# Optimization experiments

Hardware: AMD Instinct MI355X
Metric: run time of the kernel (lower is better)

The kernel has to match this reference:

```python
import jax, jax.numpy as jnp
import numpy as np

N_CONCEPTS = 32
KMEANS_ITERS = 10   # fixed Lloyd iterations (stand-in for fit-to-convergence)
CC_ITERS = 20       # label-propagation + pointer-jumping iterations (>= ~2*log2(N))


def setup_inputs() -> dict:
    key = jax.random.key(0)
    k1, k2, k3, k4 = jax.random.split(key, 4)
    B, N, F = 16, 512, 256
    x = jax.random.normal(k1, (B, N, F), dtype=jnp.float32)
    # sparse symmetric 0/1 adjacency, no self loops, avg degree ~20
    u = jax.random.uniform(k2, (B, N, N))
    a = (u < 0.02).astype(jnp.float32)
    adj = jnp.clip(a + jnp.swapaxes(a, 1, 2), 0.0, 1.0)
    adj = adj * (1.0 - jnp.eye(N, dtype=jnp.float32))
    mask = jnp.ones((B, N), dtype=bool)
    s = 1.0 / np.sqrt(F)
    W1 = jax.random.normal(k3, (F, F), jnp.float32) * s
    b1 = jnp.zeros((F,), jnp.float32)
    W2 = jax.random.normal(k4, (F, F), jnp.float32) * s
    b2 = jnp.zeros((F,), jnp.float32)
    return {"x": x, "adj": adj, "mask": mask, "W1": W1, "b1": b1, "W2": W2, "b2": b2}


def _gcn(x, adj, mask, W, b):
    # DenseGCNConv: D^-1/2 (A+I) D^-1/2 (X W) + b, masked
    N = x.shape[1]
    h = x @ W
    a = adj + jnp.eye(N, dtype=adj.dtype)
    d = jnp.clip(a.sum(-1), 1.0, None) ** -0.5
    a = d[:, :, None] * a * d[:, None, :]
    out = jnp.einsum('bij,bjf->bif', a, h) + b
    return jnp.where(mask[:, :, None], out, 0.0)


def _kmeans_fit_predict(pts, k):
    # Lloyd iterations, euclidean; deterministic init = first k points
    cent = pts[:k]
    p2 = (pts * pts).sum(-1)
    for _ in range(KMEANS_ITERS):
        d2 = p2[:, None] - 2.0 * pts @ cent.T + (cent * cent).sum(-1)[None]
        assign = jnp.argmin(d2, -1)
        sums = jax.ops.segment_sum(pts, assign, num_segments=k)
        cnt = jax.ops.segment_sum(jnp.ones_like(p2), assign, num_segments=k)
        cent = jnp.where(cnt[:, None] > 0, sums / jnp.maximum(cnt, 1.0)[:, None], cent)
    d2 = p2[:, None] - 2.0 * pts @ cent.T + (cent * cent).sum(-1)[None]
    return jnp.argmin(d2, -1)


def _components(adj_same, mask):
    # connected components of same-concept subgraph; returns 1-based cluster ids (0 = masked)
    B, N, _ = adj_same.shape
    idx = jnp.arange(N)
    labels = jnp.broadcast_to(idx[None, :], (B, N))
    A = adj_same > 0

    def step(lab, _):
        nb = jnp.where(A, lab[:, None, :], N)        # [B,N,N] neighbor labels
        lab = jnp.minimum(lab, nb.min(-1))           # hook to min neighbor
        lab = jnp.take_along_axis(lab, lab, axis=1)  # pointer jump
        lab = jnp.take_along_axis(lab, lab, axis=1)
        return lab, None

    labels, _ = jax.lax.scan(step, labels, None, length=CC_ITERS)
    is_root = mask & (labels == idx[None, :])
    ids = jnp.cumsum(is_root.astype(jnp.int32), axis=1)   # consecutive ids, 1-based at roots
    assign = jnp.take_along_axis(ids, labels, axis=1)
    return jnp.where(mask, assign, 0)


def _forward(x, adj, mask, W1, b1, W2, b2):
    B, N, F = x.shape
    h = jax.nn.relu(_gcn(x, adj, mask, W1, b1))
    h = jax.nn.relu(_gcn(h, adj, mask, W2, b2))
    # mask is all-true -> x[mask] is a flat reshape
    pts = jax.lax.stop_gradient(h.reshape(B * N, F))
    concepts = _kmeans_fit_predict(pts, N_CONCEPTS).reshape(B, N)
    adj_same = jnp.where(concepts[:, :, None] == concepts[:, None, :], adj, 0.0)
    assignments = _components(adj_same, mask)           # [B,N] in {0..N}
    seg_sum = jax.vmap(lambda v, s: jax.ops.segment_sum(v, s, num_segments=N + 1))
    x_new = seg_sum(h, assignments)[:, 1:, :]           # drop reserved cluster 0
    seg_max = jax.vmap(lambda v, s: jax.ops.segment_max(v, s, num_segments=N + 1))
    adj_r = jnp.maximum(seg_max(adj, assignments), 0.0)[:, 1:, :]                      # pool rows
    adj_new = jnp.maximum(seg_max(jnp.swapaxes(adj_r, 1, 2), assignments), 0.0)[:, 1:, :]
    adj_new = jnp.swapaxes(adj_new, 1, 2)                                              # pool cols
    num_clusters = assignments.max(-1)
    mask_new = jnp.arange(N)[None, :] < num_clusters[:, None]
    return x_new, adj_new, concepts, h, mask_new


def reference(x, adj, mask, W1, b1, W2, b2):
    return _forward(x, adj, mask, W1, b1, W2, b2)
```

## Files before the change

### kernel.cpp

```cpp
#include <hip/hip_runtime.h>
#include <cstdint>
#include <cstddef>

#define BB 16
#define NN 512
#define FF 256
#define NC 32
#define KITERS 10
#define CCITERS 20
#define MAXD 96
#define FMAXD 64

typedef __attribute__((ext_vector_type(4))) double double4_t;

__global__ __launch_bounds__(64) void build_adjbits(const float* __restrict__ adj,
                                                    unsigned long long* __restrict__ adjbits,
                                                    double* __restrict__ dinv,
                                                    unsigned short* __restrict__ nbr,
                                                    int* __restrict__ degv) {
  int i = blockIdx.x, b = blockIdx.y, lane = threadIdx.x;
  const float* row = adj + ((size_t)(b * NN + i)) * NN;
  unsigned long long lmask = (1ULL << lane) - 1ULL;
  int base = 0;
#pragma unroll
  for (int q = 0; q < 8; ++q) {
    bool pred = (row[q * 64 + lane] != 0.0f);
    unsigned long long m = __ballot(pred ? 1 : 0);
    if (lane == 0) adjbits[((size_t)(b * NN + i)) * 8 + q] = m;
    if (pred) {
      int pos = base + __popcll(m & lmask);
      if (pos < MAXD) nbr[((size_t)(b * NN + i)) * MAXD + pos] = (unsigned short)(q * 64 + lane);
    }
    base += __popcll(m);
  }
  if (lane == 0) {
    degv[b * NN + i] = base;
    double tot = (double)base + 1.0;
    dinv[b * NN + i] = 1.0 / sqrt(tot);
  }
}

__global__ __launch_bounds__(256) void gemm_scale(const float* __restrict__ X,
                                                  const float* __restrict__ W,
                                                  const double* __restrict__ dinv,
                                                  float* __restrict__ Y) {
  __shared__ float As[16][68];
  __shared__ float Bs[16][64];
  int bm = blockIdx.x, bn = blockIdx.y, b = blockIdx.z;
  int tid = threadIdx.x;
  int tx = tid & 15, ty = tid >> 4;
  const float* Xb = X + (size_t)b * NN * FF;
  float* Yb = Y + (size_t)b * NN * FF;
  double acc[4][4] = {};
  for (int kt = 0; kt < FF; kt += 16) {
    {
      int m = tid >> 2, kq = (tid & 3) * 4;
      const float4 v = *(const float4*)&Xb[(size_t)(bm * 64 + m) * FF + kt + kq];
      As[kq + 0][m] = v.x; As[kq + 1][m] = v.y; As[kq + 2][m] = v.z; As[kq + 3][m] = v.w;
    }
    {
      int k = tid >> 4, n4 = (tid & 15) * 4;
      *(float4*)&Bs[k][n4] = *(const float4*)&W[(size_t)(kt + k) * FF + bn * 64 + n4];
    }
    __syncthreads();
#pragma unroll
    for (int k = 0; k < 16; ++k) {
      float4 a = *(const float4*)&As[k][ty * 4];
      float4 bv = *(const float4*)&Bs[k][tx * 4];
      double ax = a.x, ay = a.y, az = a.z, aw = a.w;
      double bx = bv.x, by = bv.y, bz = bv.z, bw = bv.w;
      acc[0][0] += ax * bx; acc[0][1] += ax * by; acc[0][2] += ax * bz; acc[0][3] += ax * bw;
      acc[1][0] += ay * bx; acc[1][1] += ay * by; acc[1][2] += ay * bz; acc[1][3] += ay * bw;
      acc[2][0] += az * bx; acc[2][1] += az * by; acc[2][2] += az * bz; acc[2][3] += az * bw;
      acc[3][0] += aw * bx; acc[3][1] += aw * by; acc[3][2] += aw * bz; acc[3][3] += aw * bw;
    }
    __syncthreads();
  }
#pragma unroll
  for (int i = 0; i < 4; ++i) {
    int row = bm * 64 + ty * 4 + i;
    double di = dinv[b * NN + row];
    float4 v;
    v.x = (float)(di * acc[i][0]); v.y = (float)(di * acc[i][1]);
    v.z = (float)(di * acc[i][2]); v.w = (float)(di * acc[i][3]);
    *(float4*)&Yb[(size_t)row * FF + bn * 64 + tx * 4] = v;
  }
}

__global__ __launch_bounds__(256) void spmv_relu(const float* __restrict__ Y,
                                                 const unsigned short* __restrict__ nbr,
                                                 const int* __restrict__ degv,
                                                 const unsigned long long* __restrict__ adjbits,
                                                 const double* __restrict__ dinv,
                                                 const float* __restrict__ bias,
                                                 float* __restrict__ H) {
  int i = blockIdx.x, b = blockIdx.y, f = threadIdx.x;
  int row = b * NN + i;
  const float* Yb = Y + (size_t)b * NN * FF;
  double z = (double)Yb[(size_t)i * FF + f];
  int deg = degv[row];
  if (deg <= MAXD) {
    const unsigned short* lst = nbr + (size_t)row * MAXD;
    int n = 0;
    for (; n + 4 <= deg; n += 4) {
      int j0 = lst[n], j1 = lst[n + 1], j2 = lst[n + 2], j3 = lst[n + 3];
      float v0 = Yb[(size_t)j0 * FF + f];
      float v1 = Yb[(size_t)j1 * FF + f];
      float v2 = Yb[(size_t)j2 * FF + f];
      float v3 = Yb[(size_t)j3 * FF + f];
      z += (double)v0; z += (double)v1; z += (double)v2; z += (double)v3;
    }
    for (; n < deg; ++n) z += (double)Yb[(size_t)lst[n] * FF + f];
  } else {
    const unsigned long long* brow = adjbits + (size_t)row * 8;
    for (int q = 0; q < 8; ++q) {
      unsigned long long bits = brow[q];
      while (bits) {
        int j = (q << 6) + __builtin_ctzll(bits);
        bits &= bits - 1;
        z += (double)Yb[(size_t)j * FF + f];
      }
    }
  }
  double h = dinv[row] * z + (double)bias[f];
  H[((size_t)row) * FF + f] = (h > 0.0) ? (float)h : 0.0f;
}

__global__ __launch_bounds__(256) void p2cent_kernel(const float* __restrict__ pts,
                                                     double* __restrict__ p2,
                                                     double* __restrict__ cent) {
  __shared__ double red[256];
  int p = blockIdx.x, t = threadIdx.x;
  double v = (double)pts[(size_t)p * FF + t];
  if (p < NC) cent[p * FF + t] = v;
  red[t] = v * v;
  __syncthreads();
  for (int s = 128; s; s >>= 1) { if (t < s) red[t] += red[t + s]; __syncthreads(); }
  if (t == 0) p2[p] = red[0];
}

__global__ __launch_bounds__(256) void kmeans_assign(const float* __restrict__ pts,
                                                     const double* __restrict__ cent,
                                                     const double* __restrict__ p2,
                                                     int* __restrict__ assignI,
                                                     double* __restrict__ part,
                                                     int* __restrict__ cntp,
                                                     float* __restrict__ conceptsF) {
  __shared__ float ps[32][260];
  __shared__ double csT[256][35];
  __shared__ double d2s[32][33];
  __shared__ double c2s[32];
  __shared__ double want[3];
  __shared__ double probe_raw[2][2];
  __shared__ int as[32];
  __shared__ int hyp;
  int g = blockIdx.x, tid = threadIdx.x;

  for (int r = 0; r < 32; ++r) ps[r][tid] = pts[(size_t)(g * 32 + r) * FF + tid];
  for (int rep = 0; rep < 32; ++rep) csT[tid][rep] = cent[rep * FF + tid];
  __syncthreads();

  if (tid < 32) {
    double s = 0.;
    for (int k = 0; k < FF; ++k) { double cv = csT[k][tid]; s += cv * cv; }
    c2s[tid] = s;
  }

  int lane = tid & 63, w = tid >> 6;
  int prow = (w >> 1) * 16, ccol = (w & 1) * 16;
  int r16 = lane & 15, kg = lane >> 4;
  double4_t acc = {0.0, 0.0, 0.0, 0.0};
  for (int kt = 0; kt < FF; kt += 4) {
    double a = (double)ps[prow + r16][kt + kg];
    double bv = csT[kt + kg][ccol + r16];
    acc = __builtin_amdgcn_mfma_f64_16x16x4f64(a, bv, acc, 0, 0, 0);
  }
  if (tid < 2) { probe_raw[tid][0] = acc[0]; probe_raw[tid][1] = acc[1]; }
  __syncthreads();

  if (tid < 192) {
    int pw = tid >> 6;
    int pr = (pw == 2) ? 1 : 0;
    int pc = (pw == 1) ? 1 : 0;
    double partial = 0.0;
#pragma unroll
    for (int kk = 0; kk < 4; ++kk)
      partial += (double)ps[pr][lane * 4 + kk] * csT[lane * 4 + kk][pc];
    for (int off = 32; off; off >>= 1) partial += __shfl_xor(partial, off, 64);
    if (lane == 0) want[pw] = partial;
  }
  __syncthreads();
  if (tid == 0) {
    double w00 = want[0], w01 = want[1], w10 = want[2];
    double m00 = probe_raw[0][0], mA = probe_raw[1][0], mB = probe_raw[0][1];
    auto near = [](double a, double b) { return fabs(a - b) <= 1e-9 * (1.0 + fabs(b)); };
    bool ok00 = near(m00, w00);
    bool h1 = ok00 && near(mA, w01) && near(mB, w10);
    bool h2 = ok00 && near(mB, w01) && near(mA, w10);
    hyp = h1 ? 0 : (h2 ? 1 : 2);
  }
  __syncthreads();
  int hh = hyp;
  if (hh == 0) {
#pragma unroll
    for (int ii = 0; ii < 4; ++ii) {
      int row = prow + kg * 4 + ii, col = ccol + r16;
      d2s[row][col] = (p2[g * 32 + row] - 2.0 * acc[ii]) + c2s[col];
    }
  } else if (hh == 1) {
#pragma unroll
    for (int ii = 0; ii < 4; ++ii) {
      int row = prow + r16, col = ccol + kg * 4 + ii;
      d2s[row][col] = (p2[g * 32 + row] - 2.0 * acc[ii]) + c2s[col];
    }
  }
  __syncthreads();
  if (hh == 2) {
    int p0 = tid >> 4, c0 = tid & 15;
    double a00 = 0., a01 = 0., a10 = 0., a11 = 0.;
    for (int k = 0; k < FF; ++k) {
      double pa = (double)ps[p0][k], pb = (double)ps[p0 + 16][k];
      double ca = csT[k][c0], cb = csT[k][c0 + 16];
      a00 += pa * ca; a01 += pa * cb; a10 += pb * ca; a11 += pb * cb;
    }
    double pp0 = p2[g * 32 + p0], pp1 = p2[g * 32 + p0 + 16];
    double cc0 = c2s[c0], cc1 = c2s[c0 + 16];
    d2s[p0][c0]           = (pp0 - 2.0 * a00) + cc0;
    d2s[p0][c0 + 16]      = (pp0 - 2.0 * a01) + cc1;
    d2s[p0 + 16][c0]      = (pp1 - 2.0 * a10) + cc0;
    d2s[p0 + 16][c0 + 16] = (pp1 - 2.0 * a11) + cc1;
  }
  __syncthreads();

  if (tid < 32) {
    double m = d2s[tid][0];
    int idx = 0;
    for (int c = 1; c < 32; ++c) {
      double v = d2s[tid][c];
      if (v < m) { m = v; idx = c; }
    }
    as[tid] = idx;
    assignI[g * 32 + tid] = idx;
    if (conceptsF) conceptsF[g * 32 + tid] = (float)idx;
  }
  double* accm = &csT[0][0];
  for (int r = 0; r < 32; ++r) accm[r * 258 + tid] = 0.0;
  __syncthreads();
  for (int r = 0; r < 32; ++r) { int s = as[r]; accm[s * 258 + tid] += (double)ps[r][tid]; }
  for (int r = 0; r < 32; ++r) part[((size_t)r * 256 + g) * FF + tid] = accm[r * 258 + tid];
  if (tid < 32) {
    int c = 0;
    for (int r = 0; r < 32; ++r) c += (as[r] == tid) ? 1 : 0;
    cntp[tid * 256 + g] = c;
  }
}

__global__ __launch_bounds__(256) void kmeans_update(const double* __restrict__ part,
                                                     const int* __restrict__ cntp,
                                                     double* __restrict__ cent) {
  __shared__ double red[8][33];
  __shared__ int cred[256];
  int k = blockIdx.x, fc = blockIdx.y;
  int tid = threadIdx.x;
  int fl = tid & 31, gl = tid >> 5;
  int f = fc * 32 + fl;
  double s = 0.;
  for (int gg = 0; gg < 32; ++gg) {
    int g = gl + gg * 8;
    s += part[((size_t)k * 256 + g) * FF + f];
  }
  red[gl][fl] = s;
  cred[tid] = cntp[k * 256 + tid];
  __syncthreads();
  for (int q = 128; q; q >>= 1) { if (tid < q) cred[tid] += cred[tid + q]; __syncthreads(); }
  if (gl == 0) {
    double acc = 0.;
    for (int q = 0; q < 8; ++q) acc += red[q][fl];
    int cnt = cred[0];
    double v = (cnt > 0) ? (acc / (double)cnt) : cent[k * FF + f];
    cent[k * FF + f] = v;
  }
}

__global__ __launch_bounds__(64) void build_bits(const unsigned long long* __restrict__ adjbits,
                                                 const int* __restrict__ concepts,
                                                 unsigned short* __restrict__ flistT,
                                                 int* __restrict__ fdegv) {
  int i = blockIdx.x, b = blockIdx.y, lane = threadIdx.x;
  int ci = concepts[b * NN + i];
  unsigned long long lmask = (1ULL << lane) - 1ULL;
  int base = 0;
#pragma unroll
  for (int q = 0; q < 8; ++q) {
    unsigned long long wbits = adjbits[((size_t)(b * NN + i)) * 8 + q];
    bool pred = ((wbits >> lane) & 1ULL) && (concepts[b * NN + q * 64 + lane] == ci);
    unsigned long long m = __ballot(pred ? 1 : 0);
    if (pred) {
      int pos = base + __popcll(m & lmask);
      if (pos < FMAXD) flistT[((size_t)b * FMAXD + pos) * NN + i] = (unsigned short)(q * 64 + lane);
    }
    base += __popcll(m);
  }
  if (lane == 0) fdegv[b * NN + i] = base;
}

__global__ __launch_bounds__(512) void components_kernel(const unsigned short* __restrict__ flistT,
                                                         const int* __restrict__ fdegv,
                                                         int* __restrict__ comp,
                                                         float* __restrict__ maskF) {
  __shared__ unsigned short LT[FMAXD][512];
  __shared__ int lab[512];
  __shared__ int ids[512];
  int b = blockIdx.x, t = threadIdx.x;
  for (int n = 0; n < FMAXD; ++n) LT[n][t] = flistT[((size_t)b * FMAXD + n) * NN + t];
  int fd = fdegv[b * NN + t];
  if (fd > FMAXD) fd = FMAXD;
  lab[t] = t;
  __syncthreads();
  for (int it = 0; it < CCITERS; ++it) {
    int old = lab[t];
    int m = old;
    for (int n = 0; n < fd; ++n) m = min(m, lab[LT[n][t]]);
    __syncthreads();
    lab[t] = m;
    __syncthreads();
    int a = lab[m];
    __syncthreads();
    lab[t] = a;
    __syncthreads();
    int a2 = lab[a];
    __syncthreads();
    lab[t] = a2;
    int changed = (a2 != old) ? 1 : 0;
    if (__syncthreads_or(changed) == 0) break;
  }
  if (t == 0) {
    int run = 0;
    for (int i = 0; i < 512; ++i) { run += (lab[i] == i) ? 1 : 0; ids[i] = run; }
  }
  __syncthreads();
  comp[b * NN + t] = ids[lab[t]];
  maskF[b * NN + t] = (t < ids[511]) ? 1.0f : 0.0f;
}

__global__ __launch_bounds__(256) void xnew_kernel(const float* __restrict__ H,
                                                   const int* __restrict__ comp,
                                                   float* __restrict__ xnew) {
  int i = blockIdx.x, b = blockIdx.y, f = threadIdx.x;
  int s = comp[b * NN + i] - 1;
  atomicAdd(&xnew[((size_t)(b * NN + s)) * FF + f], H[((size_t)(b * NN + i)) * FF + f]);
}

__global__ __launch_bounds__(64) void adjnew_kernel(const unsigned long long* __restrict__ adjbits,
                                                    const int* __restrict__ comp,
                                                    float* __restrict__ out) {
  int b = blockIdx.y, lane = threadIdx.x;
  int i = blockIdx.x * 8 + (lane >> 3);
  int q = lane & 7;
  unsigned long long bits = adjbits[((size_t)(b * NN + i)) * 8 + q];
  if (!bits) return;
  int si = comp[b * NN + i] - 1;
  float* ob = out + (size_t)b * NN * NN;
  while (bits) {
    int j = (q << 6) + __builtin_ctzll(bits);
    bits &= bits - 1;
    int sj = comp[b * NN + j] - 1;
    ob[(size_t)si * NN + sj] = 1.0f;
  }
}

extern "C" void kernel_launch(void* const* d_in, const int* in_sizes, int n_in,
                              void* d_out, int out_size, void* d_ws, size_t ws_size,
                              hipStream_t stream) {
  (void)in_sizes; (void)n_in; (void)out_size; (void)ws_size;
  const float* x   = (const float*)d_in[0];
  const float* adj = (const float*)d_in[1];
  const float* W1 = (const float*)d_in[3];
  const float* b1 = (const float*)d_in[4];
  const float* W2 = (const float*)d_in[5];
  const float* b2 = (const float*)d_in[6];

  float* out = (float*)d_out;
  float* xnew      = out;
  float* adjnew    = out + 2097152;
  float* conceptsF = out + 6291456;
  float* hout      = out + 6299648;
  float* maskF     = out + 8396800;

  char* ws = (char*)d_ws;
  double* dinv = (double*)(ws + 0);
  float*  y    = (float*)(ws + 65536);
  float*  h1   = (float*)(ws + 8454144);
  double* cent = (double*)(ws + 16842752);
  double* p2   = (double*)(ws + 16908544);
  unsigned long long* adjbits = (unsigned long long*)(ws + 16974080);
  int* assignI = (int*)(ws + 17498368);
  int* cntp    = (int*)(ws + 17531136);
  int* comp    = (int*)(ws + 17563904);
  int* degv    = assignI;
  double* part = (double*)adjnew;
  unsigned short* nbr = (unsigned short*)xnew;
  unsigned short* flistT = (unsigned short*)h1;
  int* fdegv = (int*)(ws + 8454144 + 2097152);

  build_adjbits<<<dim3(NN, BB), 64, 0, stream>>>(adj, adjbits, dinv, nbr, degv);

  gemm_scale<<<dim3(8, 4, BB), 256, 0, stream>>>(x, W1, dinv, y);
  spmv_relu<<<dim3(NN, BB), 256, 0, stream>>>(y, nbr, degv, adjbits, dinv, b1, h1);
  gemm_scale<<<dim3(8, 4, BB), 256, 0, stream>>>(h1, W2, dinv, y);
  spmv_relu<<<dim3(NN, BB), 256, 0, stream>>>(y, nbr, degv, adjbits, dinv, b2, hout);

  hipMemsetAsync(xnew, 0, (size_t)2097152 * sizeof(float), stream);

  const float* pts = hout;
  p2cent_kernel<<<BB * NN, 256, 0, stream>>>(pts, p2, cent);
  for (int it = 0; it < KITERS; ++it) {
    kmeans_assign<<<256, 256, 0, stream>>>(pts, cent, p2, assignI, part, cntp, nullptr);
    kmeans_update<<<dim3(NC, 8), 256, 0, stream>>>(part, cntp, cent);
  }
  kmeans_assign<<<256, 256, 0, stream>>>(pts, cent, p2, assignI, part, cntp, conceptsF);

  hipMemsetAsync(adjnew, 0, (size_t)4194304 * sizeof(float), stream);

  build_bits<<<dim3(NN, BB), 64, 0, stream>>>(adjbits, assignI, flistT, fdegv);
  components_kernel<<<BB, 512, 0, stream>>>(flistT, fdegv, comp, maskF);

  xnew_kernel<<<dim3(NN, BB), 256, 0, stream>>>(hout, comp, xnew);
  adjnew_kernel<<<dim3(64, BB), 64, 0, stream>>>(adjbits, comp, adjnew);
}
```

Measured before the change: 629.2 us.

## Fuse k-means update into assign via atomics and fold p2/centroid init into SpMV

The separate kmeans_update kernel is removed. Each kmeans_it block now atomically accumulates per-cluster sums and counts into per-iteration buffers, and the next iteration computes centroids while loading them. The p2/initial-centroid computation and zeroing of those buffers move into the second spmv_relu, and build_bits is folded into components_kernel, which now uses a parallel prefix scan. This cuts about a dozen kernel launches and the partial-sum round trip through memory. In exchange it adds double-precision atomics, which make the floating-point summation order nondeterministic, and every block redundantly recomputes all centroids.

```diff
diff --git a/kernel.cpp b/kernel.cpp
--- a/kernel.cpp
+++ b/kernel.cpp
@@ -93,7 +93,11 @@
                                                  const unsigned long long* __restrict__ adjbits,
                                                  const double* __restrict__ dinv,
                                                  const float* __restrict__ bias,
-                                                 float* __restrict__ H) {
+                                                 float* __restrict__ H,
+                                                 double* __restrict__ p2out,
+                                                 double* __restrict__ cent0,
+                                                 char* __restrict__ zbuf) {
+  __shared__ double red[256];
   int i = blockIdx.x, b = blockIdx.y, f = threadIdx.x;
   int row = b * NN + i;
   const float* Yb = Y + (size_t)b * NN * FF;
@@ -123,29 +127,32 @@
     }
   }
   double h = dinv[row] * z + (double)bias[f];
-  H[((size_t)row) * FF + f] = (h > 0.0) ? (float)h : 0.0f;
-}
-
-__global__ __launch_bounds__(256) void p2cent_kernel(const float* __restrict__ pts,
-                                                     double* __restrict__ p2,
-                                                     double* __restrict__ cent) {
-  __shared__ double red[256];
-  int p = blockIdx.x, t = threadIdx.x;
-  double v = (double)pts[(size_t)p * FF + t];
-  if (p < NC) cent[p * FF + t] = v;
-  red[t] = v * v;
-  __syncthreads();
-  for (int s = 128; s; s >>= 1) { if (t < s) red[t] += red[t + s]; __syncthreads(); }
-  if (t == 0) p2[p] = red[0];
-}
-
-__global__ __launch_bounds__(256) void kmeans_assign(const float* __restrict__ pts,
-                                                     const double* __restrict__ cent,
-                                                     const double* __restrict__ p2,
-                                                     int* __restrict__ assignI,
-                                                     double* __restrict__ part,
-                                                     int* __restrict__ cntp,
-                                                     float* __restrict__ conceptsF) {
+  float hf = (h > 0.0) ? (float)h : 0.0f;
+  H[((size_t)row) * FF + f] = hf;
+
+  if (p2out) {
+    double v = (double)hf;
+    red[f] = v * v;
+    __syncthreads();
+    for (int s = 128; s; s >>= 1) { if (f < s) red[f] += red[f + s]; __syncthreads(); }
+    if (f == 0) p2out[row] = red[0];
+    if (b == 0 && i < NC) cent0[i * FF + f] = (double)hf;
+    if (b == 2 && i < 353) {
+      float4 z4 = {0.f, 0.f, 0.f, 0.f};
+      ((float4*)(zbuf + (size_t)i * 4096))[f] = z4;
+    }
+  }
+}
+
+__global__ __launch_bounds__(256) void kmeans_it(const float* __restrict__ pts,
+                                                 const double* __restrict__ cent0,
+                                                 double* __restrict__ centprev,
+                                                 double* __restrict__ cent_sum,
+                                                 int* __restrict__ cntI,
+                                                 const double* __restrict__ p2,
+                                                 int* __restrict__ assignI,
+                                                 float* __restrict__ conceptsF,
+                                                 int it) {
   __shared__ float ps[32][260];
   __shared__ double csT[256][35];
   __shared__ double d2s[32][33];
@@ -153,12 +160,23 @@
   __shared__ double want[3];
   __shared__ double probe_raw[2][2];
   __shared__ int as[32];
+  __shared__ int lcs[32];
   __shared__ int hyp;
   int g = blockIdx.x, tid = threadIdx.x;
 
   for (int r = 0; r < 32; ++r) ps[r][tid] = pts[(size_t)(g * 32 + r) * FF + tid];
-  for (int rep = 0; rep < 32; ++rep) csT[tid][rep] = cent[rep * FF + tid];
-  __syncthreads();
+  if (it == 0) {
+    for (int rep = 0; rep < 32; ++rep) csT[tid][rep] = cent0[rep * FF + tid];
+  } else {
+    for (int rep = 0; rep < 32; ++rep) {
+      int ct = cntI[(it - 1) * 32 + rep];
+      double v = (ct > 0) ? (cent_sum[((size_t)(it - 1) * 32 + rep) * FF + tid] / (double)ct)
+                          : centprev[((size_t)(it - 1) * 32 + rep) * FF + tid];
+      csT[tid][rep] = v;
+    }
+  }
+  __syncthreads();
+  if (g < 32) centprev[((size_t)it * 32 + g) * FF + tid] = csT[tid][g];
 
   if (tid < 32) {
     double s = 0.;
@@ -243,77 +261,48 @@
     assignI[g * 32 + tid] = idx;
     if (conceptsF) conceptsF[g * 32 + tid] = (float)idx;
   }
+  if (it == KITERS) return;
+
   double* accm = &csT[0][0];
   for (int r = 0; r < 32; ++r) accm[r * 258 + tid] = 0.0;
   __syncthreads();
   for (int r = 0; r < 32; ++r) { int s = as[r]; accm[s * 258 + tid] += (double)ps[r][tid]; }
-  for (int r = 0; r < 32; ++r) part[((size_t)r * 256 + g) * FF + tid] = accm[r * 258 + tid];
   if (tid < 32) {
     int c = 0;
     for (int r = 0; r < 32; ++r) c += (as[r] == tid) ? 1 : 0;
-    cntp[tid * 256 + g] = c;
-  }
-}
-
-__global__ __launch_bounds__(256) void kmeans_update(const double* __restrict__ part,
-                                                     const int* __restrict__ cntp,
-                                                     double* __restrict__ cent) {
-  __shared__ double red[8][33];
-  __shared__ int cred[256];
-  int k = blockIdx.x, fc = blockIdx.y;
-  int tid = threadIdx.x;
-  int fl = tid & 31, gl = tid >> 5;
-  int f = fc * 32 + fl;
-  double s = 0.;
-  for (int gg = 0; gg < 32; ++gg) {
-    int g = gl + gg * 8;
-    s += part[((size_t)k * 256 + g) * FF + f];
-  }
-  red[gl][fl] = s;
-  cred[tid] = cntp[k * 256 + tid];
-  __syncthreads();
-  for (int q = 128; q; q >>= 1) { if (tid < q) cred[tid] += cred[tid + q]; __syncthreads(); }
-  if (gl == 0) {
-    double acc = 0.;
-    for (int q = 0; q < 8; ++q) acc += red[q][fl];
-    int cnt = cred[0];
-    double v = (cnt > 0) ? (acc / (double)cnt) : cent[k * FF + f];
-    cent[k * FF + f] = v;
-  }
-}
-
-__global__ __launch_bounds__(64) void build_bits(const unsigned long long* __restrict__ adjbits,
-                                                 const int* __restrict__ concepts,
-                                                 unsigned short* __restrict__ flistT,
-                                                 int* __restrict__ fdegv) {
-  int i = blockIdx.x, b = blockIdx.y, lane = threadIdx.x;
-  int ci = concepts[b * NN + i];
-  unsigned long long lmask = (1ULL << lane) - 1ULL;
-  int base = 0;
-#pragma unroll
-  for (int q = 0; q < 8; ++q) {
-    unsigned long long wbits = adjbits[((size_t)(b * NN + i)) * 8 + q];
-    bool pred = ((wbits >> lane) & 1ULL) && (concepts[b * NN + q * 64 + lane] == ci);
-    unsigned long long m = __ballot(pred ? 1 : 0);
-    if (pred) {
-      int pos = base + __popcll(m & lmask);
-      if (pos < FMAXD) flistT[((size_t)b * FMAXD + pos) * NN + i] = (unsigned short)(q * 64 + lane);
-    }
-    base += __popcll(m);
-  }
-  if (lane == 0) fdegv[b * NN + i] = base;
-}
-
-__global__ __launch_bounds__(512) void components_kernel(const unsigned short* __restrict__ flistT,
-                                                         const int* __restrict__ fdegv,
+    lcs[tid] = c;
+    if (c > 0) atomicAdd(&cntI[it * 32 + tid], c);
+  }
+  __syncthreads();
+  for (int r = 0; r < 32; ++r) {
+    if (lcs[r] > 0)
+      unsafeAtomicAdd(&cent_sum[((size_t)it * 32 + r) * FF + tid], accm[r * 258 + tid]);
+  }
+}
+
+__global__ __launch_bounds__(512) void components_kernel(const unsigned long long* __restrict__ adjbits,
+                                                         const int* __restrict__ concepts,
                                                          int* __restrict__ comp,
                                                          float* __restrict__ maskF) {
+  __shared__ int cI[512];
   __shared__ unsigned short LT[FMAXD][512];
   __shared__ int lab[512];
   __shared__ int ids[512];
   int b = blockIdx.x, t = threadIdx.x;
-  for (int n = 0; n < FMAXD; ++n) LT[n][t] = flistT[((size_t)b * FMAXD + n) * NN + t];
-  int fd = fdegv[b * NN + t];
+  cI[t] = concepts[b * NN + t];
+  __syncthreads();
+  int ci = cI[t];
+  const unsigned long long* brow = adjbits + ((size_t)(b * NN + t)) * 8;
+  int fd = 0;
+#pragma unroll
+  for (int q = 0; q < 8; ++q) {
+    unsigned long long bits = brow[q];
+    while (bits) {
+      int j = (q << 6) + __builtin_ctzll(bits);
+      bits &= bits - 1;
+      if (cI[j] == ci) { if (fd < FMAXD) LT[fd][t] = (unsigned short)j; ++fd; }
+    }
+  }
   if (fd > FMAXD) fd = FMAXD;
   lab[t] = t;
   __syncthreads();
@@ -334,11 +323,14 @@
     int changed = (a2 != old) ? 1 : 0;
     if (__syncthreads_or(changed) == 0) break;
   }
-  if (t == 0) {
-    int run = 0;
-    for (int i = 0; i < 512; ++i) { run += (lab[i] == i) ? 1 : 0; ids[i] = run; }
-  }
-  __syncthreads();
+  ids[t] = (lab[t] == t) ? 1 : 0;
+  __syncthreads();
+  for (int off = 1; off < 512; off <<= 1) {
+    int v = (t >= off) ? ids[t - off] : 0;
+    __syncthreads();
+    ids[t] += v;
+    __syncthreads();
+  }
   comp[b * NN + t] = ids[lab[t]];
   maskF[b * NN + t] = (t < ids[511]) ? 1.0f : 0.0f;
 }
@@ -391,39 +383,37 @@
   double* dinv = (double*)(ws + 0);
   float*  y    = (float*)(ws + 65536);
   float*  h1   = (float*)(ws + 8454144);
-  double* cent = (double*)(ws + 16842752);
-  double* p2   = (double*)(ws + 16908544);
+  double* centprev = (double*)(ws + 8454144);
+  double* cent_sum = (double*)(ws + 9175040);
+  int*    cntI     = (int*)(ws + 9895936);
+  double* cent0 = (double*)(ws + 16842752);
+  double* p2    = (double*)(ws + 16908544);
   unsigned long long* adjbits = (unsigned long long*)(ws + 16974080);
   int* assignI = (int*)(ws + 17498368);
-  int* cntp    = (int*)(ws + 17531136);
-  int* comp    = (int*)(ws + 17563904);
+  int* comp    = (int*)(ws + 17531136);
   int* degv    = assignI;
-  double* part = (double*)adjnew;
   unsigned short* nbr = (unsigned short*)xnew;
-  unsigned short* flistT = (unsigned short*)h1;
-  int* fdegv = (int*)(ws + 8454144 + 2097152);
+
+  hipMemsetAsync(adjnew, 0, (size_t)4194304 * sizeof(float), stream);
 
   build_adjbits<<<dim3(NN, BB), 64, 0, stream>>>(adj, adjbits, dinv, nbr, degv);
 
   gemm_scale<<<dim3(8, 4, BB), 256, 0, stream>>>(x, W1, dinv, y);
-  spmv_relu<<<dim3(NN, BB), 256, 0, stream>>>(y, nbr, degv, adjbits, dinv, b1, h1);
+  spmv_relu<<<dim3(NN, BB), 256, 0, stream>>>(y, nbr, degv, adjbits, dinv, b1, h1,
+                                              nullptr, nullptr, nullptr);
   gemm_scale<<<dim3(8, 4, BB), 256, 0, stream>>>(h1, W2, dinv, y);
-  spmv_relu<<<dim3(NN, BB), 256, 0, stream>>>(y, nbr, degv, adjbits, dinv, b2, hout);
+  spmv_relu<<<dim3(NN, BB), 256, 0, stream>>>(y, nbr, degv, adjbits, dinv, b2, hout,
+                                              p2, cent0, (char*)centprev);
 
   hipMemsetAsync(xnew, 0, (size_t)2097152 * sizeof(float), stream);
 
   const float* pts = hout;
-  p2cent_kernel<<<BB * NN, 256, 0, stream>>>(pts, p2, cent);
-  for (int it = 0; it < KITERS; ++it) {
-    kmeans_assign<<<256, 256, 0, stream>>>(pts, cent, p2, assignI, part, cntp, nullptr);
-    kmeans_update<<<dim3(NC, 8), 256, 0, stream>>>(part, cntp, cent);
-  }
-  kmeans_assign<<<256, 256, 0, stream>>>(pts, cent, p2, assignI, part, cntp, conceptsF);
-
-  hipMemsetAsync(adjnew, 0, (size_t)4194304 * sizeof(float), stream);
-
-  build_bits<<<dim3(NN, BB), 64, 0, stream>>>(adjbits, assignI, flistT, fdegv);
-  components_kernel<<<BB, 512, 0, stream>>>(flistT, fdegv, comp, maskF);
+  for (int it = 0; it <= KITERS; ++it) {
+    kmeans_it<<<256, 256, 0, stream>>>(pts, cent0, centprev, cent_sum, cntI, p2,
+                                       assignI, (it == KITERS) ? conceptsF : nullptr, it);
+  }
+
+  components_kernel<<<BB, 512, 0, stream>>>(adjbits, assignI, comp, maskF);
 
   xnew_kernel<<<dim3(NN, BB), 256, 0, stream>>>(hout, comp, xnew);
   adjnew_kernel<<<dim3(64, BB), 64, 0, stream>>>(adjbits, comp, adjnew);
```

Result: faster. 614.4 us (-2.4%).
